# Kernel optimization log

Measured on AMD Instinct MI355X. Metric: run time of the kernel, lower is better.

Reference implementation:

```python
import jax, jax.numpy as jnp
import numpy as np

B, L, E = 256, 8192, 64
PS_HIGH, PS_LOW = 3, 12
THR = 1.5
WINDOW = 9
K = 5
MAXP = (L + PS_HIGH - 1) // PS_HIGH  # max possible patches per row


def setup_inputs() -> dict:
    key = jax.random.key(0)
    k1, k2, k3, k4, k5 = jax.random.split(key, 5)
    x = jax.random.randint(k1, (B, L), 0, K)  # int tokens in [0, K)
    w1 = jax.random.normal(k2, (E, 1), jnp.float32)        # Linear(1, E) weight
    b1 = jax.random.normal(k3, (E,), jnp.float32) * 0.1
    w2 = jax.random.normal(k4, (E, E), jnp.float32) / np.float32(np.sqrt(E))  # Linear(E, E) weight
    b2 = jax.random.normal(k5, (E,), jnp.float32) * 0.1
    return {"x": x, "w1": w1, "b1": b1, "w2": w2, "b2": b2}


def calc_entropy(x):
    # one-hot counts in a sliding window of size WINDOW (same as conv1d with ones kernel, groups=K)
    oh = jax.nn.one_hot(jnp.clip(x, 0, K - 1), K, dtype=jnp.float32)  # [B, L, K]
    oh = jnp.moveaxis(oh, -1, 1)                                       # [B, K, L]
    pad = WINDOW // 2
    padded = jnp.pad(oh, ((0, 0), (0, 0), (pad, pad)))                 # [B, K, L+2*pad]
    cs = jnp.cumsum(padded, axis=-1)
    csz = jnp.pad(cs, ((0, 0), (0, 0), (1, 0)))
    counts = csz[..., WINDOW:] - csz[..., :-WINDOW]                    # [B, K, L]
    total = jnp.clip(counts.sum(axis=1, keepdims=True), 1e-12, None)
    probs = counts / total
    entropy = -(probs * jnp.log2(probs + 1e-12)).sum(axis=1)           # [B, L]
    return entropy


def seg_row(cs_row, ent_row):
    # cs_row: [L+1] prefix sums of x (float); ent_row: [L] entropy
    def step(i, _):
        ent_i = ent_row[jnp.minimum(i, L - 1)]
        psize = jnp.where(ent_i > THR, PS_HIGH, PS_LOW).astype(jnp.int32)
        j = jnp.minimum(i + psize, L)
        valid = i < L
        mean = (cs_row[j] - cs_row[i]) / jnp.maximum(j - i, 1).astype(jnp.float32)
        return j, (mean, valid)

    _, (means, valids) = jax.lax.scan(step, jnp.int32(0), None, length=MAXP)
    return means, valids  # [MAXP], [MAXP]


def reference(x, w1, b1, w2, b2):
    entropy = calc_entropy(x)
    # prefix sums for O(1) per-patch means
    cs = jnp.pad(jnp.cumsum(x.astype(jnp.float32), axis=1), ((0, 0), (1, 0)))  # [B, L+1]
    means, valids = jax.vmap(seg_row)(cs, entropy)  # [B, MAXP], [B, MAXP]
    # batched tiny MLP over all candidate patches: Linear(1,E) -> ReLU -> Linear(E,E)
    h = jax.nn.relu(means[..., None] * w1[:, 0] + b1)  # [B, MAXP, E]
    vec = h @ w2.T + b2                                # [B, MAXP, E]
    m = valids[..., None].astype(jnp.float32)
    blt_features = (vec * m).sum(axis=1) / m.sum(axis=1)  # [B, E]
    return blt_features, entropy
```

## Files before the change

kernel.cpp:

```cpp
#include <hip/hip_runtime.h>
#include <math.h>


constexpr int B_ = 256;
constexpr int L_ = 8192;
constexpr int E_ = 64;
constexpr int T_ = 1024;
constexpr int PT = 8;
constexpr int CHUNK = 128;
constexpr int NCH = L_ / CHUNK;
constexpr int MAXPC = 44;

__global__ __launch_bounds__(1024)
void entropy_patcher_kernel(const int* __restrict__ x,
                            const float* __restrict__ w1,
                            const float* __restrict__ b1,
                            const float* __restrict__ w2,
                            const float* __restrict__ b2,
                            float* __restrict__ dout) {
  __shared__ __align__(16) unsigned char tok8p[8 + L_ + 8];
  __shared__ __align__(16) float csBuf[L_ + 4];
  __shared__ __align__(16) float meanbuf[NCH][MAXPC];
  __shared__ __align__(16) float pairTab[100];
  __shared__ __align__(16) unsigned char maskBytes[T_];
  __shared__ unsigned char exitT[NCH][12];
  __shared__ float rcpTab[13];
  __shared__ int cntC[NCH];
  __shared__ int waveTot[16];
  __shared__ float Sred[16][E_];
  __shared__ float partG[16][E_];
  __shared__ float avgv[E_];
  __shared__ int PcountS;

  const int tid  = threadIdx.x;
  const int lane = tid & 63;
  const int wv   = tid >> 6;
  const int b    = blockIdx.x;

  const int* xr = x + b * L_;
  float* entOut = dout + (size_t)B_ * E_ + (size_t)b * L_;

  const int4 v0 = ((const int4*)xr)[2 * tid];
  const int4 v1 = ((const int4*)xr)[2 * tid + 1];
  unsigned pw0 = (unsigned)v0.x | ((unsigned)v0.y << 8) |
                 ((unsigned)v0.z << 16) | ((unsigned)v0.w << 24);
  unsigned pw1 = (unsigned)v1.x | ((unsigned)v1.y << 8) |
                 ((unsigned)v1.z << 16) | ((unsigned)v1.w << 24);
  *(uint2*)(tok8p + 8 + 8 * tid) = make_uint2(pw0, pw1);
  if (tid == 0) *(uint2*)(tok8p) = make_uint2(~0u, ~0u);
  if (tid == 1) *(uint2*)(tok8p + 8 + L_) = make_uint2(~0u, ~0u);
  if (tid < 100) {
    int a = tid / 10, c = tid - 10 * a;
    float pa = (float)a / 9.0f, pb = (float)c / 9.0f;
    float fa = -(pa * log2f(pa + 1e-12f));
    float fb = -(pb * log2f(pb + 1e-12f));
    pairTab[tid] = fa + fb;
  }
  if (tid >= 100 && tid < 113) {
    int n = tid - 100;
    rcpTab[n] = 1.0f / (float)(n == 0 ? 1 : n);
  }
  __syncthreads();

  unsigned long long tw0 = *(const unsigned long long*)(tok8p + 8 * tid);
  unsigned long long tw1 = *(const unsigned long long*)(tok8p + 8 * tid + 8);
  unsigned long long tw2 = *(const unsigned long long*)(tok8p + 8 * tid + 16);
  unsigned code[20];
  #pragma unroll
  for (int l = 4; l < 20; ++l) {
    unsigned byte = (l < 8)  ? (unsigned)((tw0 >> (8 * l)) & 0xff)
                  : (l < 16) ? (unsigned)((tw1 >> (8 * (l - 8))) & 0xff)
                             : (unsigned)((tw2 >> (8 * (l - 16))) & 0xff);
    code[l] = (byte <= 4u) ? (1u << (6 * byte)) : 0u;
  }
  unsigned s = 0;
  #pragma unroll
  for (int l = 4; l <= 12; ++l) s += code[l];
  float entv[PT];
  #pragma unroll
  for (int q = 0; q < PT; ++q) {
    if (q) s += code[q + 12] - code[q + 3];
    unsigned a  = s & 63u,        bb = (s >> 6) & 63u, cc = (s >> 12) & 63u;
    unsigned dd = (s >> 18) & 63u, ee = (s >> 24) & 63u;
    entv[q] = pairTab[a * 10u + bb] + pairTab[cc * 10u + dd] + pairTab[ee * 10u];
  }
  if (tid == 0 || tid == T_ - 1) {
    #pragma unroll
    for (int q = 0; q < PT; ++q) {
      int p = 8 * tid + q;
      if (p < 4 || p >= L_ - 4) {
        unsigned ss = 0;
        for (int l = q + 4; l <= q + 12; ++l) ss += code[l];
        unsigned cn[5] = { ss & 63u, (ss >> 6) & 63u, (ss >> 12) & 63u,
                           (ss >> 18) & 63u, (ss >> 24) & 63u };
        float rT = 1.0f / (float)(cn[0] + cn[1] + cn[2] + cn[3] + cn[4]);
        float ent = 0.f;
        for (int k2 = 0; k2 < 5; ++k2) {
          float pr = (float)cn[k2] * rT;
          ent -= pr * log2f(pr + 1e-12f);
        }
        entv[q] = ent;
      }
    }
  }
  ((float4*)entOut)[2 * tid]     = make_float4(entv[0], entv[1], entv[2], entv[3]);
  ((float4*)entOut)[2 * tid + 1] = make_float4(entv[4], entv[5], entv[6], entv[7]);
  unsigned mbyte = 0;
  #pragma unroll
  for (int q = 0; q < PT; ++q) mbyte |= (entv[q] > 1.5f ? 1u : 0u) << q;
  maskBytes[tid] = (unsigned char)mbyte;

  int tk[8];
  #pragma unroll
  for (int j = 0; j < 4; ++j) {
    tk[j]     = (int)((pw0 >> (8 * j)) & 0xffu);
    tk[4 + j] = (int)((pw1 >> (8 * j)) & 0xffu);
  }
  int ls = tk[0] + tk[1] + tk[2] + tk[3] + tk[4] + tk[5] + tk[6] + tk[7];
  int incl = ls;
  #pragma unroll
  for (int d = 1; d < 64; d <<= 1) {
    int up = __shfl_up(incl, d, 64);
    if (lane >= d) incl += up;
  }
  if (lane == 63) waveTot[wv] = incl;
  __syncthreads();
  int base = 0;
  #pragma unroll
  for (int q = 0; q < 16; ++q) base += (q < wv) ? waveTot[q] : 0;
  float acc = (float)(base + incl - ls);
  {
    float4 c0, c1;
    c0.x = acc; acc += (float)tk[0]; c0.y = acc; acc += (float)tk[1];
    c0.z = acc; acc += (float)tk[2]; c0.w = acc; acc += (float)tk[3];
    c1.x = acc; acc += (float)tk[4]; c1.y = acc; acc += (float)tk[5];
    c1.z = acc; acc += (float)tk[6]; c1.w = acc; acc += (float)tk[7];
    ((float4*)csBuf)[2 * tid] = c0; ((float4*)csBuf)[2 * tid + 1] = c1;
    if (tid == T_ - 1) csBuf[L_] = acc;
  }

  unsigned long long m0 = 0, m1 = 0;
  if (tid < 768) {
    int c = tid & 63, o = tid >> 6;
    m0 = *(const unsigned long long*)(maskBytes + 16 * c);
    m1 = *(const unsigned long long*)(maskBytes + 16 * c + 8);
    int p = o;
    while (p < CHUNK) {
      unsigned long long mm = (p & 64) ? m1 : m0;
      p += ((mm >> (p & 63)) & 1ULL) ? 3 : 12;
    }
    exitT[c][o] = (unsigned char)(p - CHUNK);
  }
  __syncthreads();

  int myOff = 0;
  if (tid < 64) {
    const unsigned* ep = (const unsigned*)&exitT[tid][0];
    unsigned u0 = ep[0], u1 = ep[1], u2 = ep[2];
    auto nib = [](unsigned w) {
      return (w & 0xFu) | ((w >> 4) & 0xF0u) | ((w >> 8) & 0xF00u) | ((w >> 12) & 0xF000u);
    };
    unsigned long long tab = (unsigned long long)nib(u0)
                           | ((unsigned long long)nib(u1) << 16)
                           | ((unsigned long long)nib(u2) << 32);
    #pragma unroll
    for (int d = 1; d < 64; d <<= 1) {
      unsigned long long other =
          (unsigned long long)__shfl_up((long long)tab, d, 64);
      if (lane >= d) {
        unsigned long long nt = 0;
        #pragma unroll
        for (int e = 0; e < 12; ++e) {
          unsigned oe  = (unsigned)((other >> (4 * e)) & 15ULL);
          unsigned val = (unsigned)((tab >> (4 * oe)) & 15ULL);
          nt |= (unsigned long long)val << (4 * e);
        }
        tab = nt;
      }
    }
    unsigned long long prev = (unsigned long long)__shfl_up((long long)tab, 1, 64);
    myOff = (lane == 0) ? 0 : (int)(prev & 15ULL);

    int c = tid;
    int p = CHUNK * c + myOff;
    const int end = CHUNK * c + CHUNK;
    float csp = csBuf[p];
    int n = 0;
    while (p < end) {
      int lp = p - CHUNK * c;
      unsigned long long mm = (lp & 64) ? m1 : m0;
      int ps = ((mm >> (lp & 63)) & 1ULL) ? 3 : 12;
      int j = p + ps; if (j > L_) j = L_;
      float csj = csBuf[j];
      meanbuf[c][n++] = (csj - csp) * rcpTab[j - p];
      csp = csj; p = j;
    }
    cntC[c] = n;
    int tot = n;
    #pragma unroll
    for (int d2 = 32; d2; d2 >>= 1) tot += __shfl_xor(tot, d2, 64);
    if (lane == 0) PcountS = tot;
  }
  __syncthreads();

  {
    const float w1v = w1[lane];
    const float b1v = b1[lane];
    float S = 0.0f;
    for (int c = wv; c < NCH; c += 16) {
      int n = cntC[c];
      const float* mb = &meanbuf[c][0];
      int j = 0;
      for (; j + 4 <= n; j += 4) {
        float4 m4 = *((const float4*)(mb + j));
        S += fmaxf(fmaf(m4.x, w1v, b1v), 0.0f);
        S += fmaxf(fmaf(m4.y, w1v, b1v), 0.0f);
        S += fmaxf(fmaf(m4.z, w1v, b1v), 0.0f);
        S += fmaxf(fmaf(m4.w, w1v, b1v), 0.0f);
      }
      for (; j < n; ++j) S += fmaxf(fmaf(mb[j], w1v, b1v), 0.0f);
    }
    Sred[wv][lane] = S;
  }
  __syncthreads();
  if (tid < 64) {
    float sm = 0.f;
    #pragma unroll
    for (int q = 0; q < 16; ++q) sm += Sred[q][tid];
    avgv[tid] = sm / (float)PcountS;
  }
  __syncthreads();

  {
    float acc2 = 0.f;
    #pragma unroll
    for (int kk = 0; kk < 4; ++kk) {
      int k = 4 * wv + kk;
      acc2 = fmaf(avgv[k], w2[lane * 64 + k], acc2);
    }
    partG[wv][lane] = acc2;
  }
  __syncthreads();
  if (tid < 64) {
    float r = b2[tid];
    #pragma unroll
    for (int q = 0; q < 16; ++q) r += partG[q][tid];
    dout[(size_t)b * E_ + tid] = r;
  }
}

extern "C" void kernel_launch(void* const* d_in, const int* in_sizes, int n_in,
                              void* d_out, int out_size, void* d_ws, size_t ws_size,
                              hipStream_t stream) {
  const int*   x  = (const int*)d_in[0];
  const float* w1 = (const float*)d_in[1];
  const float* b1 = (const float*)d_in[2];
  const float* w2 = (const float*)d_in[3];
  const float* b2 = (const float*)d_in[4];
  float* out = (float*)d_out;
  entropy_patcher_kernel<<<B_, T_, 0, stream>>>(x, w1, b1, w2, b2, out);
}
```

Baseline: 82.68 us.

## Use 4-bit packed counts with triple/pair entropy tables and unroll segment walk

Window token counts are now packed into 4-bit fields, so entropy becomes two shared-memory lookups (a 4096-entry triple table plus a 256-entry pair table) instead of three pair lookups. Edge positions use precomputed per-window-size tables instead of calling log2f. The per-chunk patch walk computes four patch boundaries before issuing their prefix-sum loads, to overlap the dependent LDS reads. The w2 read in the final stage becomes a float4 load. In exchange it adds a 16KB table and an extra barrier at startup, which can lower occupancy.

```diff
diff --git a/kernel.cpp b/kernel.cpp
--- a/kernel.cpp
+++ b/kernel.cpp
@@ -20,8 +20,11 @@
                             float* __restrict__ dout) {
   __shared__ __align__(16) unsigned char tok8p[8 + L_ + 8];
   __shared__ __align__(16) float csBuf[L_ + 4];
+  __shared__ __align__(16) float trip[4096];
+  __shared__ __align__(16) float pair256[256];
+  __shared__ __align__(16) float fTab[16];
+  __shared__ __align__(16) float edgeF[64];
   __shared__ __align__(16) float meanbuf[NCH][MAXPC];
-  __shared__ __align__(16) float pairTab[100];
   __shared__ __align__(16) unsigned char maskBytes[T_];
   __shared__ unsigned char exitT[NCH][12];
   __shared__ float rcpTab[13];
@@ -42,6 +45,28 @@
 
   const int4 v0 = ((const int4*)xr)[2 * tid];
   const int4 v1 = ((const int4*)xr)[2 * tid + 1];
+
+  if (tid < 16) {
+    float pk = (float)tid / 9.0f;
+    fTab[tid] = (tid <= 9) ? -(pk * log2f(pk + 1e-12f)) : 0.0f;
+  } else if (tid < 80) {
+    int j = (tid - 16) >> 4, k = (tid - 16) & 15;
+    int d = j + 5;
+    float pk = (float)k / (float)d;
+    edgeF[tid - 16] = (k <= d) ? -(pk * log2f(pk + 1e-12f)) : 0.0f;
+  } else if (tid >= 96 && tid < 109) {
+    int n = tid - 96;
+    rcpTab[n] = 1.0f / (float)(n == 0 ? 1 : n);
+  }
+  __syncthreads();
+
+  #pragma unroll
+  for (int i = 0; i < 4; ++i) {
+    int t = tid + 1024 * i;
+    trip[t] = fTab[t & 15] + fTab[(t >> 4) & 15] + fTab[(t >> 8) & 15];
+  }
+  if (tid < 256) pair256[tid] = fTab[tid & 15] + fTab[tid >> 4];
+
   unsigned pw0 = (unsigned)v0.x | ((unsigned)v0.y << 8) |
                  ((unsigned)v0.z << 16) | ((unsigned)v0.w << 24);
   unsigned pw1 = (unsigned)v1.x | ((unsigned)v1.y << 8) |
@@ -49,17 +74,6 @@
   *(uint2*)(tok8p + 8 + 8 * tid) = make_uint2(pw0, pw1);
   if (tid == 0) *(uint2*)(tok8p) = make_uint2(~0u, ~0u);
   if (tid == 1) *(uint2*)(tok8p + 8 + L_) = make_uint2(~0u, ~0u);
-  if (tid < 100) {
-    int a = tid / 10, c = tid - 10 * a;
-    float pa = (float)a / 9.0f, pb = (float)c / 9.0f;
-    float fa = -(pa * log2f(pa + 1e-12f));
-    float fb = -(pb * log2f(pb + 1e-12f));
-    pairTab[tid] = fa + fb;
-  }
-  if (tid >= 100 && tid < 113) {
-    int n = tid - 100;
-    rcpTab[n] = 1.0f / (float)(n == 0 ? 1 : n);
-  }
   __syncthreads();
 
   unsigned long long tw0 = *(const unsigned long long*)(tok8p + 8 * tid);
@@ -71,18 +85,18 @@
     unsigned byte = (l < 8)  ? (unsigned)((tw0 >> (8 * l)) & 0xff)
                   : (l < 16) ? (unsigned)((tw1 >> (8 * (l - 8))) & 0xff)
                              : (unsigned)((tw2 >> (8 * (l - 16))) & 0xff);
-    code[l] = (byte <= 4u) ? (1u << (6 * byte)) : 0u;
+    if (byte > 5u) byte = 5u;
+    code[l] = 1u << (4 * byte);
   }
   unsigned s = 0;
   #pragma unroll
   for (int l = 4; l <= 12; ++l) s += code[l];
   float entv[PT];
-  #pragma unroll
-  for (int q = 0; q < PT; ++q) {
-    if (q) s += code[q + 12] - code[q + 3];
-    unsigned a  = s & 63u,        bb = (s >> 6) & 63u, cc = (s >> 12) & 63u;
-    unsigned dd = (s >> 18) & 63u, ee = (s >> 24) & 63u;
-    entv[q] = pairTab[a * 10u + bb] + pairTab[cc * 10u + dd] + pairTab[ee * 10u];
+  entv[0] = trip[s & 4095u] + pair256[(s >> 12) & 255u];
+  #pragma unroll
+  for (int q = 1; q < PT; ++q) {
+    s += code[q + 12] - code[q + 3];
+    entv[q] = trip[s & 4095u] + pair256[(s >> 12) & 255u];
   }
   if (tid == 0 || tid == T_ - 1) {
     #pragma unroll
@@ -91,15 +105,10 @@
       if (p < 4 || p >= L_ - 4) {
         unsigned ss = 0;
         for (int l = q + 4; l <= q + 12; ++l) ss += code[l];
-        unsigned cn[5] = { ss & 63u, (ss >> 6) & 63u, (ss >> 12) & 63u,
-                           (ss >> 18) & 63u, (ss >> 24) & 63u };
-        float rT = 1.0f / (float)(cn[0] + cn[1] + cn[2] + cn[3] + cn[4]);
-        float ent = 0.f;
-        for (int k2 = 0; k2 < 5; ++k2) {
-          float pr = (float)cn[k2] * rT;
-          ent -= pr * log2f(pr + 1e-12f);
-        }
-        entv[q] = ent;
+        int d = (p < 4) ? (p + 5) : (L_ + 4 - p);
+        const float* fd = &edgeF[(d - 5) * 16];
+        entv[q] = fd[ss & 15u] + fd[(ss >> 4) & 15u] + fd[(ss >> 8) & 15u]
+                + fd[(ss >> 12) & 15u] + fd[(ss >> 16) & 15u];
       }
     }
   }
@@ -153,7 +162,6 @@
   }
   __syncthreads();
 
-  int myOff = 0;
   if (tid < 64) {
     const unsigned* ep = (const unsigned*)&exitT[tid][0];
     unsigned u0 = ep[0], u1 = ep[1], u2 = ep[2];
@@ -179,21 +187,48 @@
       }
     }
     unsigned long long prev = (unsigned long long)__shfl_up((long long)tab, 1, 64);
-    myOff = (lane == 0) ? 0 : (int)(prev & 15ULL);
-
-    int c = tid;
+    int myOff = (lane == 0) ? 0 : (int)(prev & 15ULL);
+
+    const int c = tid;
+    const int end = CHUNK * c + CHUNK;
     int p = CHUNK * c + myOff;
-    const int end = CHUNK * c + CHUNK;
+    int pb = p;
+    int n = 0;
     float csp = csBuf[p];
-    int n = 0;
     while (p < end) {
-      int lp = p - CHUNK * c;
-      unsigned long long mm = (lp & 64) ? m1 : m0;
-      int ps = ((mm >> (lp & 63)) & 1ULL) ? 3 : 12;
-      int j = p + ps; if (j > L_) j = L_;
-      float csj = csBuf[j];
-      meanbuf[c][n++] = (csj - csp) * rcpTab[j - p];
-      csp = csj; p = j;
+      int j0, j1, j2, j3;
+      {
+        int pp = p;
+        int lp = pp & 127;
+        unsigned long long mm = (lp & 64) ? m1 : m0;
+        int ps = ((mm >> (lp & 63)) & 1ULL) ? 3 : 12;
+        int j = pp + ps; if (j > L_) j = L_;
+        j0 = j; pp = j;
+        bool a1 = pp < end;
+        lp = pp & 127; mm = (lp & 64) ? m1 : m0;
+        ps = ((mm >> (lp & 63)) & 1ULL) ? 3 : 12;
+        j = pp + ps; if (j > L_) j = L_;
+        j1 = a1 ? j : -1; if (a1) pp = j;
+        bool a2 = pp < end && a1;
+        lp = pp & 127; mm = (lp & 64) ? m1 : m0;
+        ps = ((mm >> (lp & 63)) & 1ULL) ? 3 : 12;
+        j = pp + ps; if (j > L_) j = L_;
+        j2 = a2 ? j : -1; if (a2) pp = j;
+        bool a3 = pp < end && a2;
+        lp = pp & 127; mm = (lp & 64) ? m1 : m0;
+        ps = ((mm >> (lp & 63)) & 1ULL) ? 3 : 12;
+        j = pp + ps; if (j > L_) j = L_;
+        j3 = a3 ? j : -1; if (a3) pp = j;
+        p = pp;
+      }
+      float f0 = csBuf[j0];
+      float f1 = csBuf[j1 < 0 ? 0 : j1];
+      float f2 = csBuf[j2 < 0 ? 0 : j2];
+      float f3 = csBuf[j3 < 0 ? 0 : j3];
+      meanbuf[c][n++] = (f0 - csp) * rcpTab[j0 - pb]; csp = f0; pb = j0;
+      if (j1 >= 0) { meanbuf[c][n++] = (f1 - csp) * rcpTab[j1 - pb]; csp = f1; pb = j1; }
+      if (j2 >= 0) { meanbuf[c][n++] = (f2 - csp) * rcpTab[j2 - pb]; csp = f2; pb = j2; }
+      if (j3 >= 0) { meanbuf[c][n++] = (f3 - csp) * rcpTab[j3 - pb]; csp = f3; pb = j3; }
     }
     cntC[c] = n;
     int tot = n;
@@ -232,12 +267,11 @@
   __syncthreads();
 
   {
-    float acc2 = 0.f;
-    #pragma unroll
-    for (int kk = 0; kk < 4; ++kk) {
-      int k = 4 * wv + kk;
-      acc2 = fmaf(avgv[k], w2[lane * 64 + k], acc2);
-    }
+    float4 wvv = *((const float4*)(w2 + lane * 64 + 4 * wv));
+    float acc2 = avgv[4 * wv + 0] * wvv.x;
+    acc2 = fmaf(avgv[4 * wv + 1], wvv.y, acc2);
+    acc2 = fmaf(avgv[4 * wv + 2], wvv.z, acc2);
+    acc2 = fmaf(avgv[4 * wv + 3], wvv.w, acc2);
     partG[wv][lane] = acc2;
   }
   __syncthreads();
```

Result: no change. 82.82 us (+0.2%).
